# Optimization experiments

Measured on AMD Instinct MI355X. Metric: run time of the kernel, lower is better.

Reference implementation:

```python
import jax, jax.numpy as jnp
from jax import lax
import numpy as np

LRELU_SLOPE = 0.01  # PyTorch LeakyReLU default
BETA = 0.25


def lrelu(x):
    return jnp.where(x >= 0, x, LRELU_SLOPE * x)


def conv2d(x, w, b, stride, pad):
    # x: [B,C,H,W], w: [Cout,Cin,k,k] (torch OIHW)
    y = lax.conv_general_dilated(x, w, (stride, stride), ((pad, pad), (pad, pad)),
                                 dimension_numbers=('NCHW', 'OIHW', 'NCHW'))
    return y + b[None, :, None, None]


def conv_transpose2d(x, w, b, stride, out_pad):
    # w: torch ConvTranspose2d weight [Cin,Cout,k,k]; implement as dilated conv
    # with spatially flipped kernel. out = (i-1)*stride + k + out_pad.
    wf = jnp.flip(w, (2, 3)).transpose(1, 0, 2, 3)  # -> [Cout,Cin,k,k]
    k = w.shape[2]
    pad = ((k - 1, k - 1 + out_pad), (k - 1, k - 1 + out_pad))
    y = lax.conv_general_dilated(x, wf, (1, 1), pad, lhs_dilation=(stride, stride),
                                 dimension_numbers=('NCHW', 'OIHW', 'NCHW'))
    return y + b[None, :, None, None]


def setup_inputs() -> dict:
    key = jax.random.key(0)
    ks = jax.random.split(key, 16)
    s = 0.05
    inp = {
        'x':   jax.random.normal(ks[0], (64, 1, 256, 256), jnp.float32),
        'ew1': jax.random.normal(ks[1], (8, 1, 4, 4), jnp.float32) * s,
        'eb1': jnp.zeros((8,), jnp.float32),
        'ew2': jax.random.normal(ks[2], (16, 8, 4, 4), jnp.float32) * s,
        'eb2': jnp.zeros((16,), jnp.float32),
        'ew3': jax.random.normal(ks[3], (32, 16, 4, 4), jnp.float32) * s,
        'eb3': jnp.zeros((32,), jnp.float32),
        'ew4': jax.random.normal(ks[4], (32, 32, 3, 3), jnp.float32) * s,
        'eb4': jnp.zeros((32,), jnp.float32),
        'ew5': jax.random.normal(ks[5], (64, 32, 1, 1), jnp.float32) * s,
        'eb5': jnp.zeros((64,), jnp.float32),
        'dw1': jax.random.normal(ks[6], (32, 64, 3, 3), jnp.float32) * s,
        'db1': jnp.zeros((32,), jnp.float32),
        'dw2': jax.random.normal(ks[7], (32, 16, 4, 4), jnp.float32) * s,
        'db2': jnp.zeros((16,), jnp.float32),
        'dw3': jax.random.normal(ks[8], (16, 8, 4, 4), jnp.float32) * s,
        'db3': jnp.zeros((8,), jnp.float32),
        'dw4': jax.random.normal(ks[9], (8, 1, 4, 4), jnp.float32) * s,
        'db4': jnp.zeros((1,), jnp.float32),
        # nn.init.uniform_(-1/K, 1/K) with K=512
        'codebook': jax.random.uniform(ks[10], (512, 64), jnp.float32,
                                       minval=-1.0 / 512, maxval=1.0 / 512),
    }
    return inp


def vqvae_forward(x, ew1, eb1, ew2, eb2, ew3, eb3, ew4, eb4, ew5, eb5,
                  dw1, db1, dw2, db2, dw3, db3, dw4, db4, codebook):
    # ---- encoder ----
    h = lrelu(conv2d(x, ew1, eb1, 2, 0))   # [B,8,127,127]
    h = lrelu(conv2d(h, ew2, eb2, 2, 0))   # [B,16,62,62]
    h = lrelu(conv2d(h, ew3, eb3, 2, 0))   # [B,32,30,30]
    h = lrelu(conv2d(h, ew4, eb4, 1, 1))   # [B,32,30,30]
    h = lrelu(conv2d(h, ew5, eb5, 1, 0))   # [B,64,30,30]
    # ---- vector quantizer ----
    lat = h.transpose(0, 2, 3, 1)                      # [B,h,w,D]
    D = lat.shape[-1]
    flat = lat.reshape(-1, D)                          # [N,D]
    # squared euclidean distances via expansion (same argmin as torch.norm)
    d2 = (jnp.sum(flat * flat, axis=1, keepdims=True)
          - 2.0 * flat @ codebook.T
          + jnp.sum(codebook * codebook, axis=1))      # [N,K]
    idx = jnp.argmin(d2, axis=1)                       # [N]
    q = codebook[idx].reshape(lat.shape)               # [B,h,w,D]
    commitment = jnp.mean((lax.stop_gradient(q) - lat) ** 2)
    embedding = jnp.mean((q - lax.stop_gradient(lat)) ** 2)
    vq_loss = commitment * BETA + embedding
    q_st = lat + lax.stop_gradient(q - lat)            # straight-through
    z = q_st.transpose(0, 3, 1, 2)                     # [B,D,h,w]
    # ---- decoder ----
    h = lrelu(conv2d(z, dw1, db1, 1, 1))               # [B,32,30,30]
    h = lrelu(conv_transpose2d(h, dw2, db2, 2, 1))     # [B,16,63,63]
    h = lrelu(conv_transpose2d(h, dw3, db3, 2, 1))     # [B,8,131,131]
    recons = jnp.tanh(conv_transpose2d(h, dw4, db4, 2, 0))  # [B,1,264,264]
    return recons, vq_loss


def reference(x, ew1, eb1, ew2, eb2, ew3, eb3, ew4, eb4, ew5, eb5,
              dw1, db1, dw2, db2, dw3, db3, dw4, db4, codebook):
    return vqvae_forward(x, ew1, eb1, ew2, eb2, ew3, eb3, ew4, eb4, ew5, eb5,
                         dw1, db1, dw2, db2, dw3, db3, dw4, db4, codebook)
```

## Files before the change

kernel.cpp:

```cpp
#include <hip/hip_runtime.h>
#include <hip/hip_bf16.h>
#include <math.h>

#define LRELU 0.01f

template<int NW>
__device__ __forceinline__ void ldw(const float* p, float* w) {
    if constexpr (NW % 4 == 0) {
#pragma unroll
        for (int u = 0; u < NW / 4; u++) {
            float4 v = *(const float4*)(p + 4 * u);
            w[4*u] = v.x; w[4*u+1] = v.y; w[4*u+2] = v.z; w[4*u+3] = v.w;
        }
    } else {
#pragma unroll
        for (int c = 0; c < NW; c++) w[c] = p[c];
    }
}

__device__ __forceinline__ void wfwd(const float* s, float* d, int CIN, int COUT,
                                     int KK, int i) {
    int co = i / (CIN * KK); int r = i - co * CIN * KK;
    int ci = r / KK; int t = r - ci * KK;
    d[(ci * KK + t) * COUT + co] = s[i];
}
__device__ __forceinline__ void wtr(const float* s, float* d, int CIN, int COUT,
                                    int KK, int i) {
    int ci = i / (COUT * KK); int r = i - ci * COUT * KK;
    int co = r / KK; int t = r - co * KK;
    d[(t * CIN + ci) * COUT + co] = s[i];
}
__global__ __launch_bounds__(256)
void prep_k(const float* e1, const float* e2, const float* e3, const float* e4,
            const float* e5, const float* d1, const float* d2, const float* d3,
            const float* d4, float* w, const float* cbp, float* hcbn,
            unsigned long long* keys, float* loss, int N) {
    int i = blockIdx.x * 256 + threadIdx.x;
    if      (i < 128)   wfwd(e1, w + 0,     1,  8, 16, i);
    else if (i < 2176)  wfwd(e2, w + 128,   8, 16, 16, i - 128);
    else if (i < 10368) wfwd(e3, w + 2176, 16, 32, 16, i - 2176);
    else if (i < 19584) wfwd(e4, w + 10368, 32, 32, 9, i - 10368);
    else if (i < 21632) wfwd(e5, w + 19584, 32, 64, 1, i - 19584);
    else if (i < 40064) wfwd(d1, w + 21632, 64, 32, 9, i - 21632);
    else if (i < 48256) wtr (d2, w + 40064, 32, 16, 16, i - 40064);
    else if (i < 50304) wtr (d3, w + 48256, 16,  8, 16, i - 48256);
    else if (i < 50432) wtr (d4, w + 50304,  8,  1, 16, i - 50304);
    else if (i < 50944) {
        int k = i - 50432;
        const float* c = cbp + k * 64;
        float s = 0.f;
#pragma unroll
        for (int d = 0; d < 64; d++) s = fmaf(c[d], c[d], s);
        hcbn[k] = 0.5f * s;
    } else if (i < 50944 + N) {
        keys[i - 50944] = 0xFFFFFFFFFFFFFFFFull;
    } else if (i == 50944 + N) {
        loss[0] = 0.f;
    }
}

template<int CIN, int COUT, int CO_BLK, int HIN, int ISTR, int HOUT, int WOUT,
         int OPLANE, int OSTR, int OPAD, int CB, int RB, int ZCONV, int ZF_CH>
__global__ __launch_bounds__(256)
void convs2_k(const float* __restrict__ in, const float* __restrict__ wt,
              const float* __restrict__ bias, float* __restrict__ out) {
    const int b = blockIdx.x, cog = blockIdx.y, tid = threadIdx.x;
    if (ZF_CH > 0 && (int)blockIdx.z >= ZCONV) {
        if (cog != 0) return;
        int i = ((int)blockIdx.z - ZCONV) * 256 + tid;
        if (i >= ZF_CH * 124) return;
        int ch = i / 124, s = i - ch * 124;
        int r, c;
        if (s < 32)      { r = 0;  c = s; }
        else if (s < 64) { r = 31; c = s - 32; }
        else { int u = s - 64; r = 1 + (u >> 1); c = (u & 1) * 31; }
        out[(size_t)(b * ZF_CH + ch) * 1024 + r * 32 + c] = 0.f;
        return;
    }
    __shared__ __align__(16) float lw[CIN * 16 * CO_BLK];
    for (int i = tid; i < CIN * 16 * CO_BLK; i += 256) {
        int row = i / CO_BLK, c = i - row * CO_BLK;
        lw[i] = wt[row * COUT + cog * CO_BLK + c];
    }
    __syncthreads();

    const int tz = blockIdx.z;
    const int cbi = tz / RB, rb = tz - cbi * RB;
    const int tx = tid & 15, ty = tid >> 4;
    const int ow0 = (cbi * 16 + tx) * 2;
    const int oh  = rb * 16 + ty;
    if (oh >= HOUT || ow0 >= WOUT) return;
    const bool p1v = (ow0 + 1) < WOUT;

    float acc[CO_BLK][2];
#pragma unroll
    for (int c = 0; c < CO_BLK; c++) {
        float bv = bias[cog * CO_BLK + c];
        acc[c][0] = bv; acc[c][1] = bv;
    }
    const float* inb = in + ((size_t)(b * CIN) * HIN + oh * 2) * ISTR + ow0 * 2;
#pragma unroll 2
    for (int ci = 0; ci < CIN; ci++) {
        const float* r = inb + (size_t)ci * HIN * ISTR;
        float4 a4[4]; float2 b2[4];
#pragma unroll
        for (int kh = 0; kh < 4; kh++) {
            a4[kh] = *(const float4*)(r + kh * ISTR);
            b2[kh] = p1v ? *(const float2*)(r + kh * ISTR + 4) : make_float2(0.f, 0.f);
        }
        const float* wr = lw + ci * 16 * CO_BLK;
#pragma unroll
        for (int kh = 0; kh < 4; kh++) {
            float x0[4] = {a4[kh].x, a4[kh].y, a4[kh].z, a4[kh].w};
            float x1[4] = {a4[kh].z, a4[kh].w, b2[kh].x, b2[kh].y};
#pragma unroll
            for (int kw = 0; kw < 4; kw++) {
                float wv[CO_BLK];
                ldw<CO_BLK>(wr + (kh * 4 + kw) * CO_BLK, wv);
#pragma unroll
                for (int c = 0; c < CO_BLK; c++) {
                    acc[c][0] = fmaf(x0[kw], wv[c], acc[c][0]);
                    acc[c][1] = fmaf(x1[kw], wv[c], acc[c][1]);
                }
            }
        }
    }
    float* ob = out + (size_t)(b * COUT + cog * CO_BLK) * OPLANE
                    + (oh + OPAD) * OSTR + ow0 + OPAD;
#pragma unroll
    for (int c = 0; c < CO_BLK; c++) {
        float v0 = acc[c][0]; v0 = (v0 >= 0.f) ? v0 : LRELU * v0;
        ob[(size_t)c * OPLANE] = v0;
        if (p1v) {
            float v1 = acc[c][1]; v1 = (v1 >= 0.f) ? v1 : LRELU * v1;
            ob[(size_t)c * OPLANE + 1] = v1;
        }
    }
}

template<int CIN, int COUT, int CO_BLK, int OPLANE, int OSTR, int OPADH, int OPADV,
         bool ZSIDE, int ZCONV, int ZF_CH>
__global__ __launch_bounds__(256)
void conv3_k(const float* __restrict__ in, const float* __restrict__ wt,
             const float* __restrict__ bias, float* __restrict__ out) {
    const int b = blockIdx.x, cog = blockIdx.y, tid = threadIdx.x;
    if (ZF_CH > 0 && (int)blockIdx.z >= ZCONV) {
        if (cog != 0) return;
        int i = ((int)blockIdx.z - ZCONV) * 256 + tid;
        if (i >= ZF_CH * 124) return;
        int ch = i / 124, s = i - ch * 124;
        int r, c;
        if (s < 32)      { r = 0;  c = s; }
        else if (s < 64) { r = 31; c = s - 32; }
        else { int u = s - 64; r = 1 + (u >> 1); c = (u & 1) * 31; }
        out[(size_t)(b * ZF_CH + ch) * 1024 + r * 32 + c] = 0.f;
        return;
    }
    __shared__ __align__(16) float lw[CIN * 9 * CO_BLK];
    for (int i = tid; i < CIN * 9 * CO_BLK; i += 256) {
        int row = i / CO_BLK, c = i - row * CO_BLK;
        lw[i] = wt[row * COUT + cog * CO_BLK + c];
    }
    __syncthreads();

    const int rb = blockIdx.z;
    const int tx = tid & 15, ty = tid >> 4;
    const int r = rb * 16 + ty;
    if (r >= 30) return;
    const int ow0 = tx * 2;
    if (tx == 15) {
        if (ZSIDE) {
#pragma unroll
            for (int c = 0; c < CO_BLK; c++) {
                float* base = out + (size_t)(b * COUT + cog * CO_BLK + c) * OPLANE
                                  + (r + OPADV) * OSTR;
                base[0] = 0.f; base[31] = 0.f; base[32] = 0.f;
            }
        }
        return;
    }
    float acc[CO_BLK][2];
#pragma unroll
    for (int c = 0; c < CO_BLK; c++) {
        float bv = bias[cog * CO_BLK + c];
        acc[c][0] = bv; acc[c][1] = bv;
    }
    const float* inb = in + ((size_t)(b * CIN) * 32 + r) * 32 + ow0;
#pragma unroll 2
    for (int ci = 0; ci < CIN; ci++) {
        const float* rr = inb + (size_t)ci * 1024;
        float2 A[3], Bv[3];
#pragma unroll
        for (int kh = 0; kh < 3; kh++) {
            A[kh]  = *(const float2*)(rr + kh * 32);
            Bv[kh] = *(const float2*)(rr + kh * 32 + 2);
        }
        const float* wr = lw + ci * 9 * CO_BLK;
#pragma unroll
        for (int kh = 0; kh < 3; kh++) {
            float x0[3] = {A[kh].x, A[kh].y, Bv[kh].x};
            float x1[3] = {A[kh].y, Bv[kh].x, Bv[kh].y};
#pragma unroll
            for (int kw = 0; kw < 3; kw++) {
                float wv[CO_BLK];
                ldw<CO_BLK>(wr + (kh * 3 + kw) * CO_BLK, wv);
#pragma unroll
                for (int c = 0; c < CO_BLK; c++) {
                    acc[c][0] = fmaf(x0[kw], wv[c], acc[c][0]);
                    acc[c][1] = fmaf(x1[kw], wv[c], acc[c][1]);
                }
            }
        }
    }
    float* ob = out + (size_t)(b * COUT + cog * CO_BLK) * OPLANE
                    + (r + OPADV) * OSTR + ow0 + OPADH;
#pragma unroll
    for (int c = 0; c < CO_BLK; c++) {
        float v0 = acc[c][0]; v0 = (v0 >= 0.f) ? v0 : LRELU * v0;
        float v1 = acc[c][1]; v1 = (v1 >= 0.f) ? v1 : LRELU * v1;
        ob[(size_t)c * OPLANE] = v0;
        ob[(size_t)c * OPLANE + 1] = v1;
    }
}

template<int CIN, int COUT, int CO_BLK>
__global__ __launch_bounds__(256)
void conv1_k(const float* __restrict__ in, const float* __restrict__ wt,
             const float* __restrict__ bias, float* __restrict__ out) {
    __shared__ __align__(16) float lw[CIN * CO_BLK];
    const int b = blockIdx.x, cog = blockIdx.y;
    for (int i = threadIdx.x; i < CIN * CO_BLK; i += 256) {
        int row = i / CO_BLK, c = i - row * CO_BLK;
        lw[i] = wt[row * COUT + cog * CO_BLK + c];
    }
    __syncthreads();

    const int px4 = threadIdx.x * 4;
    float acc[CO_BLK][4];
#pragma unroll
    for (int c = 0; c < CO_BLK; c++) {
        float bv = bias[cog * CO_BLK + c];
        acc[c][0] = bv; acc[c][1] = bv; acc[c][2] = bv; acc[c][3] = bv;
    }
#pragma unroll 4
    for (int ci = 0; ci < CIN; ci++) {
        float4 x = *(const float4*)(in + (size_t)(b * CIN + ci) * 1024 + px4);
        float wv[CO_BLK];
        ldw<CO_BLK>(lw + ci * CO_BLK, wv);
#pragma unroll
        for (int c = 0; c < CO_BLK; c++) {
            acc[c][0] = fmaf(x.x, wv[c], acc[c][0]);
            acc[c][1] = fmaf(x.y, wv[c], acc[c][1]);
            acc[c][2] = fmaf(x.z, wv[c], acc[c][2]);
            acc[c][3] = fmaf(x.w, wv[c], acc[c][3]);
        }
    }
#pragma unroll
    for (int c = 0; c < CO_BLK; c++) {
        float4 v;
        v.x = (acc[c][0] >= 0.f) ? acc[c][0] : LRELU * acc[c][0];
        v.y = (acc[c][1] >= 0.f) ? acc[c][1] : LRELU * acc[c][1];
        v.z = (acc[c][2] >= 0.f) ? acc[c][2] : LRELU * acc[c][2];
        v.w = (acc[c][3] >= 0.f) ? acc[c][3] : LRELU * acc[c][3];
        *(float4*)(out + (size_t)(b * COUT + cog * CO_BLK + c) * 1024 + px4) = v;
    }
}

template<int CIN, int COUT, int CO_BLK, int HIN, int ISTR, int HOUT, int WOUT,
         int OPLANE, int OSTR, int OPADH, int NTX, int NT,
         int ZS_CH, int ZS_H, int ZS_STR, int ZS_C0, bool DO_TANH, bool DO_LOSS>
__global__ __launch_bounds__(256)
void convtf_k(const float* __restrict__ in, const float* __restrict__ wt,
              const float* __restrict__ bias, float* __restrict__ out,
              const float* __restrict__ loss, float* __restrict__ losstgt) {
    const int b = blockIdx.x, tid = threadIdx.x;
    const int NCOG = COUT / CO_BLK;
    int zz = blockIdx.z;
    if (zz >= NCOG * NT) {
        if (DO_LOSS) {
            if (b == 0 && tid == 0)
                losstgt[0] = 1.25f * loss[0] / (57600.f * 64.f);
            return;
        }
        int i = (zz - NCOG * NT) * 256 + tid;
        if (i >= ZS_CH * ZS_H * 3) return;
        int ch = i / (ZS_H * 3); int u = i - ch * ZS_H * 3;
        int r = u / 3, c3 = u - r * 3;
        int col = (c3 == 0) ? 0 : (ZS_C0 + c3);
        out[((size_t)(b * ZS_CH + ch) * ZS_H + r) * ZS_STR + col] = 0.f;
        return;
    }
    const int cog = zz / NT, tile = zz - cog * NT;
    const int tlx = tile % NTX, tly = tile / NTX;

    __shared__ __align__(16) float lw[16 * CIN * CO_BLK];
    for (int i = tid; i < 16 * CIN * CO_BLK; i += 256) {
        int aq = i / (CIN * 4 * CO_BLK);
        int r1 = i - aq * (CIN * 4 * CO_BLK);
        int ci = r1 / (4 * CO_BLK);
        int u  = r1 - ci * (4 * CO_BLK);
        int pp = u / CO_BLK, c = u - pp * CO_BLK;
        int a = aq >> 1, q = aq & 1, py = pp >> 1, px = pp & 1;
        int tap = (py + 2 * a) * 4 + px + 2 * q;
        lw[i] = wt[((size_t)tap * CIN + ci) * COUT + cog * CO_BLK + c];
    }
    __syncthreads();

    const int SX = (WOUT + 1) >> 1, SY = (HOUT + 1) >> 1;
    const int sx0 = tlx * 32 + (tid & 15);
    const int sx1 = sx0 + 16;
    const int sy  = tly * 16 + (tid >> 4);
    const bool v0 = sx0 < SX, v1 = sx1 < SX;
    if (sy >= SY || !(v0 || v1)) return;

    const bool rvA = (sy < HIN);
    const bool rvB = (sy >= 1) && (sy <= HIN);

    float acc[2][4][CO_BLK];
#pragma unroll
    for (int s = 0; s < 2; s++)
#pragma unroll
        for (int o = 0; o < 4; o++)
#pragma unroll
            for (int c = 0; c < CO_BLK; c++)
                acc[s][o][c] = bias[cog * CO_BLK + c];

    const float* base = in + (size_t)(b * CIN) * HIN * ISTR;
#pragma unroll 2
    for (int ci = 0; ci < CIN; ci++) {
        const float* rowA = base + (size_t)ci * HIN * ISTR + (size_t)sy * ISTR;
        const float* rowB = rowA - ISTR;
        float rA0x = 0.f, rA0y = 0.f, rA1x = 0.f, rA1y = 0.f;
        float rB0x = 0.f, rB0y = 0.f, rB1x = 0.f, rB1y = 0.f;
        if (rvA) {
            if (v0) { rA0x = rowA[sx0]; rA0y = rowA[sx0 + 1]; }
            if (v1) { rA1x = rowA[sx1]; rA1y = rowA[sx1 + 1]; }
        }
        if (rvB) {
            if (v0) { rB0x = rowB[sx0]; rB0y = rowB[sx0 + 1]; }
            if (v1) { rB1x = rowB[sx1]; rB1y = rowB[sx1 + 1]; }
        }
#pragma unroll
        for (int a = 0; a < 2; a++) {
#pragma unroll
            for (int q = 0; q < 2; q++) {
                float iv0 = q ? (a ? rB0x : rA0x) : (a ? rB0y : rA0y);
                float iv1 = q ? (a ? rB1x : rA1x) : (a ? rB1y : rA1y);
                const float* wp = lw + (size_t)((a * 2 + q) * CIN + ci) * (4 * CO_BLK);
                float wv[4 * CO_BLK];
                ldw<4 * CO_BLK>(wp, wv);
#pragma unroll
                for (int o = 0; o < 4; o++)
#pragma unroll
                    for (int c = 0; c < CO_BLK; c++) {
                        acc[0][o][c] = fmaf(iv0, wv[o * CO_BLK + c], acc[0][o][c]);
                        acc[1][o][c] = fmaf(iv1, wv[o * CO_BLK + c], acc[1][o][c]);
                    }
            }
        }
    }
#pragma unroll
    for (int s = 0; s < 2; s++) {
        if (s ? !v1 : !v0) continue;
        const int sxx = s ? sx1 : sx0;
#pragma unroll
        for (int py = 0; py < 2; py++) {
            int oh = 2 * sy + py;
            if (oh >= HOUT) continue;
#pragma unroll
            for (int px = 0; px < 2; px++) {
                int ow = 2 * sxx + px;
                if (ow >= WOUT) continue;
                float* ob = out + (size_t)(b * COUT + cog * CO_BLK) * OPLANE
                                + (size_t)oh * OSTR + ow + OPADH;
#pragma unroll
                for (int c = 0; c < CO_BLK; c++) {
                    float v = acc[s][py * 2 + px][c];
                    if (DO_TANH) v = tanhf(v);
                    else v = (v >= 0.f) ? v : LRELU * v;
                    ob[(size_t)c * OPLANE] = v;
                }
            }
        }
    }
}

__global__ __launch_bounds__(256)
void vq_argmin_k(const float* __restrict__ lat, const float* __restrict__ cb,
                 const float* __restrict__ hcbn,
                 unsigned long long* __restrict__ keys, int kofs) {
    const int pb = blockIdx.x;
    if (pb >= 225) return;
    __shared__ float4 scb4[1024];
    __shared__ float  shn[64];
    const int tid = threadIdx.x;
    const int dq  = tid & 3;
    const int pg  = tid >> 2;
    const int kbase = (blockIdx.y + kofs) * 64;
    const int posbase = pb * 256;

    const float4* src = (const float4*)(cb + (size_t)kbase * 64);
#pragma unroll
    for (int i = 0; i < 4; i++) scb4[tid + 256 * i] = src[tid + 256 * i];
    if (tid < 64) shn[tid] = hcbn[kbase + tid];

    float l[4][16];
    int   pidx[4];
#pragma unroll
    for (int j = 0; j < 4; j++) {
        int pos = posbase + pg + 64 * j;
        pidx[j] = pos;
        int b = pos / 900, p = pos - b * 900;
        int oh = p / 30, ow = p - oh * 30;
        int pp = 33 + oh * 32 + ow;
        const float* lb = lat + ((size_t)b * 64 + dq * 16) * 1024 + pp;
#pragma unroll
        for (int i = 0; i < 16; i++) l[j][i] = lb[i * 1024];
    }
    __syncthreads();

    float best[4] = {3.4e38f, 3.4e38f, 3.4e38f, 3.4e38f};
    int   bi[4]   = {0, 0, 0, 0};
#pragma unroll 2
    for (int k0 = 0; k0 < 64; k0++) {
        float4 c0 = scb4[k0 * 16 + dq * 4 + 0];
        float4 c1 = scb4[k0 * 16 + dq * 4 + 1];
        float4 c2 = scb4[k0 * 16 + dq * 4 + 2];
        float4 c3 = scb4[k0 * 16 + dq * 4 + 3];
        float hn = shn[k0];
#pragma unroll
        for (int j = 0; j < 4; j++) {
            float dot = 0.f;
            dot = fmaf(l[j][0],  c0.x, dot); dot = fmaf(l[j][1],  c0.y, dot);
            dot = fmaf(l[j][2],  c0.z, dot); dot = fmaf(l[j][3],  c0.w, dot);
            dot = fmaf(l[j][4],  c1.x, dot); dot = fmaf(l[j][5],  c1.y, dot);
            dot = fmaf(l[j][6],  c1.z, dot); dot = fmaf(l[j][7],  c1.w, dot);
            dot = fmaf(l[j][8],  c2.x, dot); dot = fmaf(l[j][9],  c2.y, dot);
            dot = fmaf(l[j][10], c2.z, dot); dot = fmaf(l[j][11], c2.w, dot);
            dot = fmaf(l[j][12], c3.x, dot); dot = fmaf(l[j][13], c3.y, dot);
            dot = fmaf(l[j][14], c3.z, dot); dot = fmaf(l[j][15], c3.w, dot);
            float full = dot + __shfl_xor(dot, 1);
            full += __shfl_xor(full, 2);
            float score = hn - full;
            if (score < best[j]) { best[j] = score; bi[j] = kbase + k0; }
        }
    }
    if (dq == 0) {
#pragma unroll
        for (int j = 0; j < 4; j++) {
            unsigned u = __float_as_uint(best[j]);
            u = ((int)u < 0) ? ~u : (u | 0x80000000u);
            unsigned long long key = ((unsigned long long)u << 32) | (unsigned)bi[j];
            atomicMin(&keys[pidx[j]], key);
        }
    }
}

__global__ __launch_bounds__(256)
void vq_finalize_k(const float* __restrict__ lat, const float* __restrict__ cb,
                   const unsigned long long* __restrict__ keys,
                   float* __restrict__ z, float* __restrict__ loss_acc, int B) {
    int gid = blockIdx.x * 256 + threadIdx.x;
    const int N = B * 900;
    float myloss = 0.f;
    if (gid < N) {
        int b = gid / 900, p = gid - b * 900;
        int oh = p / 30, ow = p - oh * 30;
        int pp = 33 + oh * 32 + ow;
        int idx = (int)(unsigned)(keys[gid] & 0xFFFFFFFFull);
        const float4* crow = (const float4*)(cb + (size_t)idx * 64);
        const float* lrow = lat + (size_t)b * 64 * 1024 + pp;
        float*       zrow = z   + (size_t)b * 64 * 1024 + pp;
#pragma unroll
        for (int i = 0; i < 16; i++) {
            float4 cv = crow[i];
            float lv0 = lrow[(4 * i + 0) * 1024];
            float lv1 = lrow[(4 * i + 1) * 1024];
            float lv2 = lrow[(4 * i + 2) * 1024];
            float lv3 = lrow[(4 * i + 3) * 1024];
            zrow[(4 * i + 0) * 1024] = cv.x;
            zrow[(4 * i + 1) * 1024] = cv.y;
            zrow[(4 * i + 2) * 1024] = cv.z;
            zrow[(4 * i + 3) * 1024] = cv.w;
            float d0 = cv.x - lv0, d1 = cv.y - lv1, d2 = cv.z - lv2, d3 = cv.w - lv3;
            myloss = fmaf(d0, d0, myloss);
            myloss = fmaf(d1, d1, myloss);
            myloss = fmaf(d2, d2, myloss);
            myloss = fmaf(d3, d3, myloss);
        }
    }
    __shared__ float red[256];
    red[threadIdx.x] = myloss;
    __syncthreads();
    for (int s = 128; s > 0; s >>= 1) {
        if ((int)threadIdx.x < s) red[threadIdx.x] += red[threadIdx.x + s];
        __syncthreads();
    }
    if (threadIdx.x == 0) atomicAdd(loss_acc, red[0]);
}

static inline int nblk(long long total) { return (int)((total + 255) / 256); }

extern "C" void kernel_launch(void* const* d_in, const int* in_sizes, int n_in,
                              void* d_out, int out_size, void* d_ws, size_t ws_size,
                              hipStream_t stream) {
    const float* x   = (const float*)d_in[0];
    const float* ew1 = (const float*)d_in[1];  const float* eb1 = (const float*)d_in[2];
    const float* ew2 = (const float*)d_in[3];  const float* eb2 = (const float*)d_in[4];
    const float* ew3 = (const float*)d_in[5];  const float* eb3 = (const float*)d_in[6];
    const float* ew4 = (const float*)d_in[7];  const float* eb4 = (const float*)d_in[8];
    const float* ew5 = (const float*)d_in[9];  const float* eb5 = (const float*)d_in[10];
    const float* dw1 = (const float*)d_in[11]; const float* db1 = (const float*)d_in[12];
    const float* dw2 = (const float*)d_in[13]; const float* db2 = (const float*)d_in[14];
    const float* dw3 = (const float*)d_in[15]; const float* db3 = (const float*)d_in[16];
    const float* dw4 = (const float*)d_in[17]; const float* db4 = (const float*)d_in[18];
    const float* cb  = (const float*)d_in[19];
    float* out = (float*)d_out;

    const int B = in_sizes[0] / (256 * 256);
    const int N = B * 900;

    char* ws = (char*)d_ws;
    float* A  = (float*)(ws);
    float* Bb = (float*)(ws + 34873344);
    unsigned long long* keys = (unsigned long long*)(ws + 51904512);
    float* hcbn = (float*)(ws + 52365312);
    float* loss = (float*)(ws + 52367360);
    float* wtb  = (float*)(ws + 52367616);
    float* ew1t = wtb;          float* ew2t = wtb + 128;
    float* ew3t = wtb + 2176;   float* ew4t = wtb + 10368;
    float* ew5t = wtb + 19584;  float* dw1t = wtb + 21632;
    float* dw2t = wtb + 40064;  float* dw3t = wtb + 48256;
    float* dw4t = wtb + 50304;

    prep_k<<<nblk(50945 + N), 256, 0, stream>>>(ew1, ew2, ew3, ew4, ew5,
                                                dw1, dw2, dw3, dw4, wtb,
                                                cb, hcbn, keys, loss, N);

    convs2_k<1, 8, 8, 256, 256, 127, 127, 127 * 128, 128, 0, 4, 8, 32, 0>
        <<<dim3(B, 1, 32), 256, 0, stream>>>(x, ew1t, eb1, A);
    convs2_k<8, 16, 4, 127, 128, 62, 62, 62 * 64, 64, 0, 2, 4, 8, 0>
        <<<dim3(B, 4, 8), 256, 0, stream>>>(A, ew2t, eb2, Bb);
    convs2_k<16, 32, 4, 62, 64, 30, 30, 1024, 32, 1, 1, 2, 2, 32>
        <<<dim3(B, 8, 18), 256, 0, stream>>>(Bb, ew3t, eb3, A);
    conv3_k<32, 32, 4, 1024, 32, 1, 1, false, 2, 64>
        <<<dim3(B, 8, 33), 256, 0, stream>>>(A, ew4t, eb4, Bb);
    conv1_k<32, 64, 4><<<dim3(B, 16, 1), 256, 0, stream>>>(Bb, ew5t, eb5, A);

    vq_argmin_k<<<dim3(232, 4), 256, 0, stream>>>(A, cb, hcbn, keys, 0);
    vq_argmin_k<<<dim3(232, 4), 256, 0, stream>>>(A, cb, hcbn, keys, 4);
    vq_finalize_k<<<nblk(N), 256, 0, stream>>>(A, cb, keys, Bb, loss, B);

    conv3_k<64, 32, 4, 30 * 34, 34, 1, 0, true, 2, 0>
        <<<dim3(B, 8, 2), 256, 0, stream>>>(Bb, dw1t, db1, A);
    convtf_k<32, 16, 4, 30, 34, 63, 63, 63 * 66, 66, 1, 1, 2,
             16, 63, 66, 63, false, false>
        <<<dim3(B, 1, 20), 256, 0, stream>>>(A, dw2t, db2, Bb, nullptr, nullptr);
    convtf_k<16, 8, 8, 63, 66, 129, 129, 129 * 132, 132, 1, 3, 15,
             8, 129, 132, 129, false, false>
        <<<dim3(B, 1, 28), 256, 0, stream>>>(Bb, dw3t, db3, A, nullptr, nullptr);
    convtf_k<8, 1, 1, 129, 132, 260, 260, 67600, 260, 0, 5, 45,
             0, 1, 1, 0, true, true>
        <<<dim3(B, 1, 46), 256, 0, stream>>>(A, dw4t, db4, out, loss,
                                             out + (out_size - 1));
}
```

Before: 479.5 us.

## Replace decoder first conv with codebook-tap lookup table indexed by VQ indices

The quantized latent only takes one of 512 codebook vectors, so the first decoder 3x3 conv is precomputed per codebook entry and tap into a table U (512x9x32, plus a zero row for padding). A new kernel sums nine table rows indexed by the per-pixel codebook index instead of running a 64-channel conv. vq_finalize now writes only index maps rather than the full z tensor. Zero-border initialisation moves into prep_k. This trades the conv FLOPs and the z write for a small table build and gather loads.

```diff
diff --git a/kernel.cpp b/kernel.cpp
--- a/kernel.cpp
+++ b/kernel.cpp
@@ -34,7 +34,7 @@
 void prep_k(const float* e1, const float* e2, const float* e3, const float* e4,
             const float* e5, const float* d1, const float* d2, const float* d3,
             const float* d4, float* w, const float* cbp, float* hcbn,
-            unsigned long long* keys, float* loss, int N) {
+            unsigned long long* keys, float* loss, int* idxm, int N) {
     int i = blockIdx.x * 256 + threadIdx.x;
     if      (i < 128)   wfwd(e1, w + 0,     1,  8, 16, i);
     else if (i < 2176)  wfwd(e2, w + 128,   8, 16, 16, i - 128);
@@ -56,7 +56,30 @@
         keys[i - 50944] = 0xFFFFFFFFFFFFFFFFull;
     } else if (i == 50944 + N) {
         loss[0] = 0.f;
-    }
+    } else if (i < 50945 + N + 64 * 124) {
+        int j = i - (50945 + N);
+        int b2 = j / 124, s = j - b2 * 124;
+        int r, c;
+        if (s < 32)      { r = 0;  c = s; }
+        else if (s < 64) { r = 31; c = s - 32; }
+        else { int u = s - 64; r = 1 + (u >> 1); c = (u & 1) * 31; }
+        idxm[b2 * 1024 + r * 32 + c] = 512;
+    }
+}
+
+__global__ __launch_bounds__(256)
+void ubuild_k(const float* __restrict__ w, const float* __restrict__ cb,
+              float* __restrict__ U) {
+    int g = blockIdx.x * 256 + threadIdx.x;
+    if (g >= 513 * 288) return;
+    if (g >= 512 * 288) { U[g] = 0.f; return; }
+    int k = g / 288, rem = g - k * 288;
+    const float* cr = cb + k * 64;
+    float s = 0.f;
+#pragma unroll 4
+    for (int ci = 0; ci < 64; ci++)
+        s = fmaf(w[ci * 288 + rem], cr[ci], s);
+    U[g] = s;
 }
 
 template<int CIN, int COUT, int CO_BLK, int HIN, int ISTR, int HOUT, int WOUT,
@@ -139,23 +162,11 @@
 }
 
 template<int CIN, int COUT, int CO_BLK, int OPLANE, int OSTR, int OPADH, int OPADV,
-         bool ZSIDE, int ZCONV, int ZF_CH>
+         bool ZSIDE>
 __global__ __launch_bounds__(256)
 void conv3_k(const float* __restrict__ in, const float* __restrict__ wt,
              const float* __restrict__ bias, float* __restrict__ out) {
     const int b = blockIdx.x, cog = blockIdx.y, tid = threadIdx.x;
-    if (ZF_CH > 0 && (int)blockIdx.z >= ZCONV) {
-        if (cog != 0) return;
-        int i = ((int)blockIdx.z - ZCONV) * 256 + tid;
-        if (i >= ZF_CH * 124) return;
-        int ch = i / 124, s = i - ch * 124;
-        int r, c;
-        if (s < 32)      { r = 0;  c = s; }
-        else if (s < 64) { r = 31; c = s - 32; }
-        else { int u = s - 64; r = 1 + (u >> 1); c = (u & 1) * 31; }
-        out[(size_t)(b * ZF_CH + ch) * 1024 + r * 32 + c] = 0.f;
-        return;
-    }
     __shared__ __align__(16) float lw[CIN * 9 * CO_BLK];
     for (int i = tid; i < CIN * 9 * CO_BLK; i += 256) {
         int row = i / CO_BLK, c = i - row * CO_BLK;
@@ -263,6 +274,52 @@
         v.z = (acc[c][2] >= 0.f) ? acc[c][2] : LRELU * acc[c][2];
         v.w = (acc[c][3] >= 0.f) ? acc[c][3] : LRELU * acc[c][3];
         *(float4*)(out + (size_t)(b * COUT + cog * CO_BLK + c) * 1024 + px4) = v;
+    }
+}
+
+__global__ __launch_bounds__(256)
+void d1tab_k(const int* __restrict__ idxm, const float* __restrict__ U,
+             const float* __restrict__ bias, float* __restrict__ out) {
+    const int b = blockIdx.x, cog = blockIdx.y, rt = blockIdx.z;
+    const int tx = threadIdx.x & 31, ty = threadIdx.x >> 5;
+    const int r = rt * 8 + ty;
+    if (r >= 30) return;
+    if (tx >= 30) {
+        if (tx == 31) {
+#pragma unroll
+            for (int c = 0; c < 16; c++) {
+                float* base = out + (size_t)(b * 32 + cog * 16 + c) * 1020 + r * 34;
+                base[0] = 0.f; base[31] = 0.f; base[32] = 0.f;
+            }
+        }
+        return;
+    }
+    const int* im = idxm + b * 1024 + r * 32 + tx;
+    float acc[16];
+#pragma unroll
+    for (int c = 0; c < 16; c++) acc[c] = bias[cog * 16 + c];
+#pragma unroll
+    for (int kh = 0; kh < 3; kh++) {
+        int i0 = im[kh * 32 + 0];
+        int i1 = im[kh * 32 + 1];
+        int i2 = im[kh * 32 + 2];
+        const float4* u0 = (const float4*)(U + ((size_t)i0 * 9 + kh * 3 + 0) * 32 + cog * 16);
+        const float4* u1 = (const float4*)(U + ((size_t)i1 * 9 + kh * 3 + 1) * 32 + cog * 16);
+        const float4* u2 = (const float4*)(U + ((size_t)i2 * 9 + kh * 3 + 2) * 32 + cog * 16);
+#pragma unroll
+        for (int q = 0; q < 4; q++) {
+            float4 a = u0[q], bb = u1[q], cc = u2[q];
+            acc[4*q+0] += (a.x + bb.x) + cc.x;
+            acc[4*q+1] += (a.y + bb.y) + cc.y;
+            acc[4*q+2] += (a.z + bb.z) + cc.z;
+            acc[4*q+3] += (a.w + bb.w) + cc.w;
+        }
+    }
+    float* ob = out + (size_t)(b * 32 + cog * 16) * 1020 + r * 34 + tx + 1;
+#pragma unroll
+    for (int c = 0; c < 16; c++) {
+        float v = acc[c]; v = (v >= 0.f) ? v : LRELU * v;
+        ob[(size_t)c * 1020] = v;
     }
 }
 
@@ -459,7 +516,7 @@
 __global__ __launch_bounds__(256)
 void vq_finalize_k(const float* __restrict__ lat, const float* __restrict__ cb,
                    const unsigned long long* __restrict__ keys,
-                   float* __restrict__ z, float* __restrict__ loss_acc, int B) {
+                   int* __restrict__ idxm, float* __restrict__ loss_acc, int B) {
     int gid = blockIdx.x * 256 + threadIdx.x;
     const int N = B * 900;
     float myloss = 0.f;
@@ -468,9 +525,9 @@
         int oh = p / 30, ow = p - oh * 30;
         int pp = 33 + oh * 32 + ow;
         int idx = (int)(unsigned)(keys[gid] & 0xFFFFFFFFull);
+        idxm[b * 1024 + pp] = idx;
         const float4* crow = (const float4*)(cb + (size_t)idx * 64);
         const float* lrow = lat + (size_t)b * 64 * 1024 + pp;
-        float*       zrow = z   + (size_t)b * 64 * 1024 + pp;
 #pragma unroll
         for (int i = 0; i < 16; i++) {
             float4 cv = crow[i];
@@ -478,10 +535,6 @@
             float lv1 = lrow[(4 * i + 1) * 1024];
             float lv2 = lrow[(4 * i + 2) * 1024];
             float lv3 = lrow[(4 * i + 3) * 1024];
-            zrow[(4 * i + 0) * 1024] = cv.x;
-            zrow[(4 * i + 1) * 1024] = cv.y;
-            zrow[(4 * i + 2) * 1024] = cv.z;
-            zrow[(4 * i + 3) * 1024] = cv.w;
             float d0 = cv.x - lv0, d1 = cv.y - lv1, d2 = cv.z - lv2, d3 = cv.w - lv3;
             myloss = fmaf(d0, d0, myloss);
             myloss = fmaf(d1, d1, myloss);
@@ -527,15 +580,18 @@
     float* hcbn = (float*)(ws + 52365312);
     float* loss = (float*)(ws + 52367360);
     float* wtb  = (float*)(ws + 52367616);
+    int*   idxm = (int*)(ws + 52572160);
+    float* U    = (float*)(ws + 52834304);
     float* ew1t = wtb;          float* ew2t = wtb + 128;
     float* ew3t = wtb + 2176;   float* ew4t = wtb + 10368;
     float* ew5t = wtb + 19584;  float* dw1t = wtb + 21632;
     float* dw2t = wtb + 40064;  float* dw3t = wtb + 48256;
     float* dw4t = wtb + 50304;
 
-    prep_k<<<nblk(50945 + N), 256, 0, stream>>>(ew1, ew2, ew3, ew4, ew5,
-                                                dw1, dw2, dw3, dw4, wtb,
-                                                cb, hcbn, keys, loss, N);
+    prep_k<<<nblk(50945 + N + 64 * 124), 256, 0, stream>>>(
+        ew1, ew2, ew3, ew4, ew5, dw1, dw2, dw3, dw4, wtb,
+        cb, hcbn, keys, loss, idxm, N);
+    ubuild_k<<<nblk(513 * 288), 256, 0, stream>>>(dw1t, cb, U);
 
     convs2_k<1, 8, 8, 256, 256, 127, 127, 127 * 128, 128, 0, 4, 8, 32, 0>
         <<<dim3(B, 1, 32), 256, 0, stream>>>(x, ew1t, eb1, A);
@@ -543,16 +599,15 @@
         <<<dim3(B, 4, 8), 256, 0, stream>>>(A, ew2t, eb2, Bb);
     convs2_k<16, 32, 4, 62, 64, 30, 30, 1024, 32, 1, 1, 2, 2, 32>
         <<<dim3(B, 8, 18), 256, 0, stream>>>(Bb, ew3t, eb3, A);
-    conv3_k<32, 32, 4, 1024, 32, 1, 1, false, 2, 64>
-        <<<dim3(B, 8, 33), 256, 0, stream>>>(A, ew4t, eb4, Bb);
+    conv3_k<32, 32, 4, 1024, 32, 1, 1, false>
+        <<<dim3(B, 8, 2), 256, 0, stream>>>(A, ew4t, eb4, Bb);
     conv1_k<32, 64, 4><<<dim3(B, 16, 1), 256, 0, stream>>>(Bb, ew5t, eb5, A);
 
     vq_argmin_k<<<dim3(232, 4), 256, 0, stream>>>(A, cb, hcbn, keys, 0);
     vq_argmin_k<<<dim3(232, 4), 256, 0, stream>>>(A, cb, hcbn, keys, 4);
-    vq_finalize_k<<<nblk(N), 256, 0, stream>>>(A, cb, keys, Bb, loss, B);
-
-    conv3_k<64, 32, 4, 30 * 34, 34, 1, 0, true, 2, 0>
-        <<<dim3(B, 8, 2), 256, 0, stream>>>(Bb, dw1t, db1, A);
+    vq_finalize_k<<<nblk(N), 256, 0, stream>>>(A, cb, keys, idxm, loss, B);
+
+    d1tab_k<<<dim3(B, 2, 4), 256, 0, stream>>>(idxm, U, db1, A);
     convtf_k<32, 16, 4, 30, 34, 63, 63, 63 * 66, 66, 1, 1, 2,
              16, 63, 66, 63, false, false>
         <<<dim3(B, 1, 20), 256, 0, stream>>>(A, dw2t, db2, Bb, nullptr, nullptr);
```

Result: faster. 420.1 us (-12.4%).
